# Optimization experiments

Hardware: AMD Instinct MI355X
Metric: run time of the kernel (lower is better)

Reference implementation:

```python
import jax, jax.numpy as jnp
import numpy as np

NUM_CAPS = 8
IN_CH = 768
OUT_CH = 64  # == num_routes
BATCH = 16384


def setup_inputs() -> dict:
    key = jax.random.key(0)
    ks = jax.random.split(key, 9)
    lim = 1.0 / np.sqrt(IN_CH)  # torch Linear default init range
    inp = {
        'img_emb': jax.random.normal(ks[0], (BATCH, IN_CH), jnp.float32),
        'capt_emb': jax.random.normal(ks[1], (BATCH, IN_CH), jnp.float32),
        'dct_emb': jax.random.normal(ks[2], (BATCH, IN_CH), jnp.float32),
        'W_img': jax.random.uniform(ks[3], (NUM_CAPS, OUT_CH, IN_CH), jnp.float32, -lim, lim),
        'b_img': jax.random.uniform(ks[4], (NUM_CAPS, OUT_CH), jnp.float32, -lim, lim),
        'W_capt': jax.random.uniform(ks[5], (NUM_CAPS, OUT_CH, IN_CH), jnp.float32, -lim, lim),
        'b_capt': jax.random.uniform(ks[6], (NUM_CAPS, OUT_CH), jnp.float32, -lim, lim),
        'W_dct': jax.random.uniform(ks[7], (NUM_CAPS, OUT_CH, IN_CH), jnp.float32, -lim, lim),
        'b_dct': jax.random.uniform(ks[8], (NUM_CAPS, OUT_CH), jnp.float32, -lim, lim),
    }
    return inp


def _project(x, W, b):
    # x: [B, I]; W: [C, R, I]; b: [C, R] -> [B, R, C]
    # torch: per-capsule Linear y = x @ W_c.T + b_c, viewed [B, R, 1], cat on last dim
    y = jnp.einsum('bi,cri->brc', x, W) + b.T[None]  # [B, R, C]
    return y


def _squash(u, epsilon=1e-07):
    sq = jnp.sum(u * u, axis=-1, keepdims=True)  # [B, 3R, 1]
    safe_norm = jnp.sqrt(sq + epsilon)
    return sq * u / ((1.0 + sq) * safe_norm)


def reference(img_emb, capt_emb, dct_emb, W_img, b_img, W_capt, b_capt, W_dct, b_dct):
    u_img = _project(img_emb, W_img, b_img)      # [B, 64, 8]
    u_capt = _project(capt_emb, W_capt, b_capt)  # [B, 64, 8]
    u_dct = _project(dct_emb, W_dct, b_dct)      # [B, 64, 8]
    combined = jnp.concatenate([u_img, u_capt, u_dct], axis=1)  # [B, 192, 8]
    return _squash(combined)
```

## Files before the change

kernel.cpp:

```cpp
#include <hip/hip_runtime.h>

typedef __attribute__((ext_vector_type(8))) short short8;
typedef __attribute__((ext_vector_type(4))) float floatx4;
typedef __attribute__((ext_vector_type(4))) unsigned int uintx4;

#if __has_builtin(__builtin_amdgcn_cvt_pk_bf16_f32)
typedef __attribute__((ext_vector_type(2))) __bf16 bf16x2;
__device__ __forceinline__ unsigned int pk_bf16(float a, float b) {
  bf16x2 v = __builtin_amdgcn_cvt_pk_bf16_f32(a, b);
  return __builtin_bit_cast(unsigned int, v);
}
#else
__device__ __forceinline__ unsigned int bf16_1(float f) {
  unsigned int u = __builtin_bit_cast(unsigned int, f);
  return (u + 0x7fffu + ((u >> 16) & 1u)) >> 16;
}
__device__ __forceinline__ unsigned int pk_bf16(float a, float b) {
  return bf16_1(a) | (bf16_1(b) << 16);
}
#endif


__global__ __launch_bounds__(256) void prep_w(
    const float* __restrict__ Wi, const float* __restrict__ Wc, const float* __restrict__ Wd,
    const float* __restrict__ bi, const float* __restrict__ bc, const float* __restrict__ bd,
    uintx4* __restrict__ Bprep, float* __restrict__ biasPrep) {
  const int t = blockIdx.x * 256 + threadIdx.x;
  const int l = t & 63;
  const int frag = t >> 6;
  const int nt = frag & 3;
  const int q = frag >> 2;
  const int ks = q % 24;
  const int q2 = q / 24;
  const int h = q2 & 7;
  const int mod = q2 >> 3;
  const int n16 = h * 4 + nt;
  const float* __restrict__ W = (mod == 0) ? Wi : ((mod == 1) ? Wc : Wd);

  const int n = n16 * 16 + (l & 15);
  const int r = n >> 3;
  const int c = n & 7;
  const int i0 = ks * 32 + (l >> 4) * 8;
  const float* src = W + (size_t)(c * 64 + r) * 768 + i0;
  floatx4 f0 = *(const floatx4*)(src);
  floatx4 f1 = *(const floatx4*)(src + 4);
  uintx4 p;
  p.x = pk_bf16(f0.x, f0.y);
  p.y = pk_bf16(f0.z, f0.w);
  p.z = pk_bf16(f1.x, f1.y);
  p.w = pk_bf16(f1.z, f1.w);
  Bprep[(size_t)frag * 64 + l] = p;

  if (t < 1536) {
    const int m2 = t >> 9;
    const int nn = t & 511;
    const float* bb = (m2 == 0) ? bi : ((m2 == 1) ? bc : bd);
    biasPrep[t] = bb[(nn & 7) * 64 + (nn >> 3)];
  }
}

#define LOADA(aa, kk)                                                        \
  {                                                                          \
    _Pragma("unroll") for (int mt = 0; mt < 2; ++mt)                         \
        aa[mt] = Afr[((kk) * 2 + mt) * 64 +                                  \
                     ((ln ^ (((kk) * 4 + quad) & 15)) + (quad << 4))];       \
  }

#define LOADB(bb, kk)                                                        \
  {                                                                          \
    _Pragma("unroll") for (int n2 = 0; n2 < 4; ++n2)                         \
        bb[n2] = bbase[((kk) * 4 + n2) * 64];                                \
  }

#define COMP(aa, bb)                                                     \
  {                                                                      \
    _Pragma("unroll") for (int mt = 0; mt < 2; ++mt)                     \
    {                                                                    \
      short8 af = __builtin_bit_cast(short8, aa[mt]);                    \
      _Pragma("unroll") for (int n2 = 0; n2 < 4; ++n2)                   \
          acc[mt][n2] = __builtin_amdgcn_mfma_f32_16x16x32_bf16(         \
              af, __builtin_bit_cast(short8, bb[n2]), acc[mt][n2], 0, 0, \
              0);                                                        \
    }                                                                    \
  }

__global__ __launch_bounds__(512, 4) void caps_fused(
    const float* __restrict__ x0, const float* __restrict__ x1, const float* __restrict__ x2,
    const uintx4* __restrict__ Bprep, const float* __restrict__ biasPrep,
    float* __restrict__ out) {
  __shared__ unsigned long long As64[48 * 128];

  const int tid = threadIdx.x;
  const int bx0 = blockIdx.x;
  const int bx = (bx0 & 7) * 192 + (bx0 >> 3);
  const int mod = bx >> 9;
  const int bm = bx & 511;
  const float* __restrict__ X = (mod == 0) ? x0 : ((mod == 1) ? x1 : x2);

  const float* src = X + (size_t)bm * 32 * 768;
#pragma unroll
  for (int i = 0; i < 12; ++i) {
    const int idx = i * 2048 + tid * 4;
    floatx4 f = *(const floatx4*)(src + idx);
    const int m = (unsigned)idx / 768u;
    const int k = idx - m * 768;
    const int ks = k >> 5;
    const int kk = k & 31;
    const int qk = kk >> 3;
    const int jh = (kk >> 2) & 1;
    const int mt = m >> 4;
    const int lnn = m & 15;
    const int p = (ks * 4 + qk) & 15;
    const int slot = (lnn ^ p) + (qk << 4);
    unsigned long long w =
        ((unsigned long long)pk_bf16(f.z, f.w) << 32) | pk_bf16(f.x, f.y);
    As64[(((ks * 2 + mt) * 64 + slot) << 1) + jh] = w;
  }
  __syncthreads();

  const int lane = tid & 63;
  const int ln = lane & 15;
  const int quad = lane >> 4;
  const int wv = tid >> 6;

  const uintx4* Afr = (const uintx4*)As64;
  const uintx4* bbase = Bprep + (size_t)(mod * 8 + wv) * (96 * 64) + lane;

  floatx4 acc[2][4] = {};
  uintx4 a0[2], a1[2], a2[2], b0[4], b1[4], b2[4];

  LOADA(a0, 0); LOADB(b0, 0);
  LOADA(a1, 1); LOADB(b1, 1);
  LOADA(a2, 2); LOADB(b2, 2);
#pragma unroll
  for (int it = 0; it < 7; ++it) {
    const int s = 3 * it;
    COMP(a0, b0);
    LOADA(a0, s + 3); LOADB(b0, s + 3);
    COMP(a1, b1);
    LOADA(a1, s + 4); LOADB(b1, s + 4);
    COMP(a2, b2);
    LOADA(a2, s + 5); LOADB(b2, s + 5);
  }
  COMP(a0, b0);
  COMP(a1, b1);
  COMP(a2, b2);

  const int col0 = mod * 512 + wv * 64 + ln;
  float bias[4];
#pragma unroll
  for (int n2 = 0; n2 < 4; ++n2) bias[n2] = biasPrep[col0 + n2 * 16];

#pragma unroll
  for (int mt = 0; mt < 2; ++mt) {
    float* opm = out + (size_t)(bm * 32 + mt * 16 + quad * 4) * 1536 + col0;
#pragma unroll
    for (int jj = 0; jj < 4; ++jj) {
      float* opj = opm + jj * 1536;
#pragma unroll
      for (int n2 = 0; n2 < 4; ++n2) {
        float u = acc[mt][n2][jj] + bias[n2];
        float s = u * u;
        s += __shfl_xor(s, 1);
        s += __shfl_xor(s, 2);
        s += __shfl_xor(s, 4);
#if __has_builtin(__builtin_amdgcn_rsqf) && __has_builtin(__builtin_amdgcn_rcpf)
        float sc = s * __builtin_amdgcn_rsqf(s + 1e-7f) *
                   __builtin_amdgcn_rcpf(1.0f + s);
#else
        float sc = s / ((1.0f + s) * sqrtf(s + 1e-7f));
#endif
        opj[n2 * 16] = u * sc;
      }
    }
  }
}

extern "C" void kernel_launch(void* const* d_in, const int* in_sizes, int n_in,
                              void* d_out, int out_size, void* d_ws, size_t ws_size,
                              hipStream_t stream) {
  const float* ximg = (const float*)d_in[0];
  const float* xcapt = (const float*)d_in[1];
  const float* xdct = (const float*)d_in[2];
  const float* Wi = (const float*)d_in[3];
  const float* bi = (const float*)d_in[4];
  const float* Wc = (const float*)d_in[5];
  const float* bc = (const float*)d_in[6];
  const float* Wd = (const float*)d_in[7];
  const float* bd = (const float*)d_in[8];

  uintx4* Bprep = (uintx4*)d_ws;
  float* biasPrep = (float*)((char*)d_ws + 2304 * 1024);

  hipLaunchKernelGGL(prep_w, dim3(576), dim3(256), 0, stream,
                     Wi, Wc, Wd, bi, bc, bd, Bprep, biasPrep);
  hipLaunchKernelGGL(caps_fused, dim3(1536), dim3(512), 0, stream,
                     ximg, xcapt, xdct, (const uintx4*)Bprep, biasPrep,
                     (float*)d_out);
}
```

Measured before the change: 84.94 us.

## Split K across two wave groups per block and reduce partials via LDS

Doubles the block to 1024 threads: the 16 waves split the 24 K-steps into two halves of 12, and each half accumulates partial MFMA results for the same output tile. The upper half writes its partials to a new 64KB LDS buffer, and after a barrier the lower half adds them in and runs the bias, squash and store epilogue. The aim is more waves in flight to hide latency and a shorter serial MFMA chain per wave. The cost is higher LDS use, which may lower occupancy, plus an extra barrier and half the waves idling during the epilogue.

```diff
diff --git a/kernel.cpp b/kernel.cpp
--- a/kernel.cpp
+++ b/kernel.cpp
@@ -59,11 +59,12 @@
   }
 }
 
-#define LOADA(aa, kk)                                                        \
+#define LOADA(aa, kk)       \
   {                                                                          \
     _Pragma("unroll") for (int mt = 0; mt < 2; ++mt)                         \
-        aa[mt] = Afr[((kk) * 2 + mt) * 64 +                                  \
-                     ((ln ^ (((kk) * 4 + quad) & 15)) + (quad << 4))];       \
+        aa[mt] = Afr[((khb + (kk)) * 2 + mt) * 64 +                          \
+                     ((ln ^ (((khb + (kk)) * 4 + quad) & 15)) +              \
+                      (quad << 4))];                                         \
   }
 
 #define LOADB(bb, kk)                                                        \
@@ -84,11 +85,12 @@
     }                                                                    \
   }
 
-__global__ __launch_bounds__(512, 4) void caps_fused(
+__global__ __launch_bounds__(1024, 4) void caps_fused(
     const float* __restrict__ x0, const float* __restrict__ x1, const float* __restrict__ x2,
     const uintx4* __restrict__ Bprep, const float* __restrict__ biasPrep,
     float* __restrict__ out) {
   __shared__ unsigned long long As64[48 * 128];
+  __shared__ floatx4 Ex[8 * 8 * 64];
 
   const int tid = threadIdx.x;
   const int bx0 = blockIdx.x;
@@ -99,8 +101,8 @@
 
   const float* src = X + (size_t)bm * 32 * 768;
 #pragma unroll
-  for (int i = 0; i < 12; ++i) {
-    const int idx = i * 2048 + tid * 4;
+  for (int i = 0; i < 6; ++i) {
+    const int idx = i * 4096 + tid * 4;
     floatx4 f = *(const floatx4*)(src + idx);
     const int m = (unsigned)idx / 768u;
     const int k = idx - m * 768;
@@ -122,55 +124,71 @@
   const int ln = lane & 15;
   const int quad = lane >> 4;
   const int wv = tid >> 6;
+  const int cg = wv & 7;
+  const int kh = wv >> 3;
+  const int khb = kh * 12;
 
   const uintx4* Afr = (const uintx4*)As64;
-  const uintx4* bbase = Bprep + (size_t)(mod * 8 + wv) * (96 * 64) + lane;
+  const uintx4* bbase =
+      Bprep + (size_t)(mod * 8 + cg) * (96 * 64) + khb * 4 * 64 + lane;
 
   floatx4 acc[2][4] = {};
-  uintx4 a0[2], a1[2], a2[2], b0[4], b1[4], b2[4];
+  uintx4 a0[2], a1[2], b0[4], b1[4];
 
   LOADA(a0, 0); LOADB(b0, 0);
-  LOADA(a1, 1); LOADB(b1, 1);
-  LOADA(a2, 2); LOADB(b2, 2);
-#pragma unroll
-  for (int it = 0; it < 7; ++it) {
-    const int s = 3 * it;
+#pragma unroll
+  for (int j = 0; j < 6; ++j) {
+    const int s = 2 * j;
+    LOADA(a1, s + 1); LOADB(b1, s + 1);
     COMP(a0, b0);
-    LOADA(a0, s + 3); LOADB(b0, s + 3);
+    if (j != 5) { LOADA(a0, s + 2); LOADB(b0, s + 2); }
     COMP(a1, b1);
-    LOADA(a1, s + 4); LOADB(b1, s + 4);
-    COMP(a2, b2);
-    LOADA(a2, s + 5); LOADB(b2, s + 5);
-  }
-  COMP(a0, b0);
-  COMP(a1, b1);
-  COMP(a2, b2);
-
-  const int col0 = mod * 512 + wv * 64 + ln;
-  float bias[4];
-#pragma unroll
-  for (int n2 = 0; n2 < 4; ++n2) bias[n2] = biasPrep[col0 + n2 * 16];
-
-#pragma unroll
-  for (int mt = 0; mt < 2; ++mt) {
-    float* opm = out + (size_t)(bm * 32 + mt * 16 + quad * 4) * 1536 + col0;
-#pragma unroll
-    for (int jj = 0; jj < 4; ++jj) {
-      float* opj = opm + jj * 1536;
+  }
+
+  if (kh == 1) {
+#pragma unroll
+    for (int mt = 0; mt < 2; ++mt)
+#pragma unroll
+      for (int n2 = 0; n2 < 4; ++n2)
+        Ex[((mt * 4 + n2) * 8 + cg) * 64 + lane] = acc[mt][n2];
+  }
+  __syncthreads();
+  if (kh == 0) {
+#pragma unroll
+    for (int mt = 0; mt < 2; ++mt)
 #pragma unroll
       for (int n2 = 0; n2 < 4; ++n2) {
-        float u = acc[mt][n2][jj] + bias[n2];
-        float s = u * u;
-        s += __shfl_xor(s, 1);
-        s += __shfl_xor(s, 2);
-        s += __shfl_xor(s, 4);
+        floatx4 o = Ex[((mt * 4 + n2) * 8 + cg) * 64 + lane];
+        acc[mt][n2].x += o.x; acc[mt][n2].y += o.y;
+        acc[mt][n2].z += o.z; acc[mt][n2].w += o.w;
+      }
+
+    const int col0 = mod * 512 + cg * 64 + ln;
+    float bias[4];
+#pragma unroll
+    for (int n2 = 0; n2 < 4; ++n2) bias[n2] = biasPrep[col0 + n2 * 16];
+
+#pragma unroll
+    for (int mt = 0; mt < 2; ++mt) {
+      float* opm = out + (size_t)(bm * 32 + mt * 16 + quad * 4) * 1536 + col0;
+#pragma unroll
+      for (int jj = 0; jj < 4; ++jj) {
+        float* opj = opm + jj * 1536;
+#pragma unroll
+        for (int n2 = 0; n2 < 4; ++n2) {
+          float u = acc[mt][n2][jj] + bias[n2];
+          float s = u * u;
+          s += __shfl_xor(s, 1);
+          s += __shfl_xor(s, 2);
+          s += __shfl_xor(s, 4);
 #if __has_builtin(__builtin_amdgcn_rsqf) && __has_builtin(__builtin_amdgcn_rcpf)
-        float sc = s * __builtin_amdgcn_rsqf(s + 1e-7f) *
-                   __builtin_amdgcn_rcpf(1.0f + s);
+          float sc = s * __builtin_amdgcn_rsqf(s + 1e-7f) *
+                     __builtin_amdgcn_rcpf(1.0f + s);
 #else
-        float sc = s / ((1.0f + s) * sqrtf(s + 1e-7f));
+          float sc = s / ((1.0f + s) * sqrtf(s + 1e-7f));
 #endif
-        opj[n2 * 16] = u * sc;
+          opj[n2 * 16] = u * sc;
+        }
       }
     }
   }
@@ -194,7 +212,7 @@
 
   hipLaunchKernelGGL(prep_w, dim3(576), dim3(256), 0, stream,
                      Wi, Wc, Wd, bi, bc, bd, Bprep, biasPrep);
-  hipLaunchKernelGGL(caps_fused, dim3(1536), dim3(512), 0, stream,
+  hipLaunchKernelGGL(caps_fused, dim3(1536), dim3(1024), 0, stream,
                      ximg, xcapt, xdct, (const uintx4*)Bprep, biasPrep,
                      (float*)d_out);
 }
```

After: 106.7 us. 1.26x slower.
